# Performance work log

Hardware: AMD Instinct MI355X
Metric: run time of the kernel (lower is better)

The kernel has to match this reference:

```python
import jax, jax.numpy as jnp
import numpy as np

TEMPERATURE = 0.1
BASE_TEMPERATURE = 0.07
EPS = 1e-10


def setup_inputs() -> dict:
    key = jax.random.key(0)
    k1, k2 = jax.random.split(key)
    # feats_: [total_classes=64, n_view=128, feat_dim=256] sampled anchor features
    feats_ = jax.random.normal(k1, (64, 128, 256), dtype=jnp.float32)
    # labels_: class id per anchor group (21-class dataset -> repeats across groups)
    labels_ = jax.random.randint(k2, (64,), 0, 21, dtype=jnp.int32)
    return {"feats_": feats_, "labels_": labels_}


def reference(feats_, labels_):
    anchor_num, n_view, d = feats_.shape
    N = anchor_num * n_view
    # torch.cat(torch.unbind(feats_, dim=1), dim=0): view-major flattening
    cf = jnp.transpose(feats_, (1, 0, 2)).reshape(N, d)  # [N, d]
    # labels for the flattened ordering (mask.repeat tiles the [A,A] eq-mask)
    big_labels = jnp.tile(labels_, n_view)  # [N]

    logits = jnp.matmul(cf, cf.T) / TEMPERATURE  # [N, N]
    logits = logits - jax.lax.stop_gradient(jnp.max(logits, axis=1, keepdims=True))

    mask = (big_labels[:, None] == big_labels[None, :]).astype(jnp.float32)
    neg_mask = 1.0 - mask                       # negatives BEFORE removing diagonal
    mask = mask * (1.0 - jnp.eye(N, dtype=jnp.float32))  # positives exclude self

    exp_logits = jnp.exp(logits)
    neg_logits = jnp.sum(exp_logits * neg_mask, axis=1, keepdims=True)  # [N, 1]
    log_prob = logits - jnp.log(exp_logits + neg_logits + EPS)
    mean_log_prob_pos = jnp.sum(mask * log_prob, axis=1) / jnp.sum(mask, axis=1)
    loss = jnp.mean(-(TEMPERATURE / BASE_TEMPERATURE) * mean_log_prob_pos)
    return loss
```

## Files before the change

kernel.cpp:

```cpp
#include <hip/hip_runtime.h>
#include <hip/hip_bf16.h>

#define N_ROWS 8192
#define DIM 256
#define NANCH 64
#define NVIEW 128
#define NPART 8

typedef __attribute__((ext_vector_type(8))) short bf16x8;
typedef __attribute__((ext_vector_type(4))) float f32x4;
typedef __attribute__((ext_vector_type(16))) float f32x16;
typedef __attribute__((ext_vector_type(4))) float float4v;
typedef __attribute__((ext_vector_type(4))) unsigned short ushort4v;

__device__ __forceinline__ unsigned short f2bf(float x) {
  union { float f; unsigned int u; } c; c.f = x;
  unsigned int u = c.u;
  unsigned int r = (u + 0x7fffu + ((u >> 16) & 1u)) >> 16;
  return (unsigned short)r;
}

__device__ __forceinline__ float bf2f(unsigned short b) {
  union { unsigned int u; float f; } c; c.u = ((unsigned int)b) << 16;
  return c.f;
}

__device__ __forceinline__ void gload_lds16(const void* g, void* l) {
  __builtin_amdgcn_global_load_lds(
      (const __attribute__((address_space(1))) unsigned int*)g,
      (__attribute__((address_space(3))) unsigned int*)l, 16, 0, 0);
}

__global__ void cast_diag_kernel(const float4v* __restrict__ in,
                                 ushort4v* __restrict__ out,
                                 float* __restrict__ diag) {
  const int w = threadIdx.x >> 6;
  const int l = threadIdx.x & 63;
  const int row = blockIdx.x * 4 + w;
  const float s = 3.16227766016838f;
  float4v v = in[row * 64 + l];
  ushort4v o;
  o.x = f2bf(v.x * s);
  o.y = f2bf(v.y * s);
  o.z = f2bf(v.z * s);
  o.w = f2bf(v.w * s);
  out[row * 64 + l] = o;
  float c0 = bf2f(o.x), c1 = bf2f(o.y), c2 = bf2f(o.z), c3 = bf2f(o.w);
  float ss = c0 * c0 + c1 * c1 + c2 * c2 + c3 * c3;
#pragma unroll
  for (int st = 1; st < 64; st <<= 1) ss += __shfl_xor(ss, st);
  if (l == 0) diag[row] = ss;
}

__global__ __launch_bounds__(512, 2) void pcl_negsum(
    const unsigned short* __restrict__ Xb, const int* __restrict__ labels,
    const float* __restrict__ diag, float* __restrict__ ns_partial) {
  const int bx = blockIdx.x;
  const int rbp = bx & 31;
  const int part = bx >> 5;
  const int abase = part * 8;
  const int tid = threadIdx.x;
  const int wid = tid >> 6;
  const int lane = tid & 63;
  const int l31 = lane & 31;
  const int khalf = lane >> 5;
  const int rg = wid >> 1;
  const int cg = wid & 1;
  const int R0 = rbp * 256;

  __shared__ __align__(16) unsigned short ring[4 * 64 * DIM];
  __shared__ float sdiag[256];
  __shared__ float nsacc[256];
  __shared__ int slab[NANCH];

  if (tid < NANCH) slab[tid] = labels[tid];
  if (tid < 256) { sdiag[tid] = diag[R0 + tid]; nsacc[tid] = 0.f; }
  __syncthreads();
  const int myLab = slab[rbp * 2 + (rg >> 1)];

  bf16x8 afrag[2][16];
#pragma unroll
  for (int ri = 0; ri < 2; ++ri) {
#pragma unroll
    for (int ks = 0; ks < 16; ++ks) {
      const unsigned short* p =
          Xb + (size_t)(R0 + rg * 64 + ri * 32 + l31) * DIM + ks * 16 + khalf * 8;
      afrag[ri][ks] = *(const bf16x8*)p;
    }
  }
#pragma unroll
  for (int ri = 0; ri < 2; ++ri)
#pragma unroll
    for (int ks = 0; ks < 16; ++ks) asm volatile("" : "+v"(afrag[ri][ks]));

  float thr;
  {
    float d = sdiag[rg * 64 + lane];
#pragma unroll
    for (int st = 1; st < 64; st <<= 1) d = fminf(d, __shfl_xor(d, st));
    thr = d - 40.f;
  }

  char* const L0 = (char*)&ring[0];

#define STAGE(H)                                                                \
  do {                                                                          \
    const unsigned short* _s =                                                  \
        Xb + (size_t)((abase + ((H) >> 1)) * NVIEW + ((H) & 1) * 64 + lane) *   \
                 DIM + wid * 8;                                                 \
    char* _d = L0 + ((H) & 3) * 32768 + wid * 1024;                             \
    gload_lds16(_s, _d);                                                        \
    gload_lds16(_s + 64, _d + 8192);                                            \
    gload_lds16(_s + 128, _d + 16384);                                          \
    gload_lds16(_s + 192, _d + 24576);                                          \
  } while (0)

  STAGE(0);
  STAGE(1);
  STAGE(2);

#define ITER(S, VN)                                                             \
  do {                                                                          \
    if ((S) + 3 < 16) STAGE((S) + 3);                                           \
    asm volatile("s_waitcnt vmcnt(" #VN ")");                                   \
    __builtin_amdgcn_sched_barrier(0);                                          \
    __builtin_amdgcn_s_barrier();                                               \
    __builtin_amdgcn_sched_barrier(0);                                          \
    const char* _sb =                                                           \
        L0 + ((S) & 3) * 32768 + khalf * 1024 + cg * 512 + l31 * 16;            \
    f32x16 a0A = {}, a0B = {}, a1A = {}, a1B = {};                              \
    __builtin_amdgcn_s_setprio(1);                                              \
    _Pragma("unroll") for (int ks = 0; ks < 8; ++ks) {                          \
      bf16x8 b0 = *(const bf16x8*)(_sb + ks * 2048);                            \
      bf16x8 b1 = *(const bf16x8*)(_sb + (ks + 8) * 2048);                      \
      a0A = __builtin_amdgcn_mfma_f32_32x32x16_bf16(afrag[0][ks], b0, a0A, 0, 0, 0); \
      a1A = __builtin_amdgcn_mfma_f32_32x32x16_bf16(afrag[1][ks], b0, a1A, 0, 0, 0); \
      a0B = __builtin_amdgcn_mfma_f32_32x32x16_bf16(afrag[0][ks + 8], b1, a0B, 0, 0, 0); \
      a1B = __builtin_amdgcn_mfma_f32_32x32x16_bf16(afrag[1][ks + 8], b1, a1B, 0, 0, 0); \
    }                                                                           \
    __builtin_amdgcn_s_setprio(0);                                              \
    if (slab[abase + ((S) >> 1)] != myLab) {                                    \
      f32x16 c0 = a0A + a0B;                                                    \
      f32x16 c1 = a1A + a1B;                                                    \
      float vmax = fmaxf(c0[0], c1[0]);                                         \
      _Pragma("unroll") for (int r = 1; r < 16; ++r)                            \
          vmax = fmaxf(vmax, fmaxf(c0[r], c1[r]));                              \
      if (__builtin_expect(__any(vmax > thr), 0)) {                             \
        _Pragma("unroll") for (int t2 = 0; t2 < 2; ++t2) {                      \
          _Pragma("unroll") for (int r = 0; r < 16; ++r) {                      \
            const int rloc = (r & 3) + 8 * (r >> 2) + 4 * khalf;                \
            const int row = rg * 64 + t2 * 32 + rloc;                           \
            float v = t2 ? c1[r] : c0[r];                                       \
            float mr = sdiag[row];                                              \
            float e = (v > mr - 40.f) ? __expf(v - mr) : 0.f;                   \
            _Pragma("unroll") for (int st = 1; st < 32; st <<= 1)               \
                e += __shfl_xor(e, st);                                         \
            if (l31 == 0) atomicAdd(&nsacc[row], e);                            \
          }                                                                     \
        }                                                                       \
      }                                                                         \
    }                                                                           \
    __builtin_amdgcn_s_barrier();                                               \
  } while (0)

  ITER(0, 12);  ITER(1, 12);  ITER(2, 12);  ITER(3, 12);
  ITER(4, 12);  ITER(5, 12);  ITER(6, 12);  ITER(7, 12);
  ITER(8, 12);  ITER(9, 12);  ITER(10, 12); ITER(11, 12);
  ITER(12, 12); ITER(13, 8);  ITER(14, 4);  ITER(15, 0);

#undef ITER
#undef STAGE

  __syncthreads();
  if (tid < 256) ns_partial[part * N_ROWS + R0 + tid] = nsacc[tid];
}

__global__ __launch_bounds__(512, 4) void pcl_pos(
    const unsigned short* __restrict__ Xb, const int* __restrict__ labels,
    const float* __restrict__ diag, const float* __restrict__ ns_partial,
    float* __restrict__ partials) {
  const int blk = blockIdx.x;
  const int r0 = blk * 32;
  const int tid = threadIdx.x;
  const int wid = tid >> 6;
  const int lane = tid & 63;
  const int lo = lane & 15;
  const int hi = lane >> 4;
  const int cq = wid & 3;
  const int bq = wid >> 2;

  __shared__ int slab[NANCH];
  __shared__ float sred[8][32];
  __shared__ float smf[32];
  __shared__ float snsf[32];
  __shared__ float slog[32];
  __shared__ int poslist[NANCH];
  __shared__ int scnt;

  if (tid < NANCH) slab[tid] = labels[tid];
  if (tid >= 64 && tid < 96) {
    int r = tid - 64;
    smf[r] = diag[r0 + r];
    float s = 0.f;
#pragma unroll
    for (int p = 0; p < NPART; ++p) s += ns_partial[p * N_ROWS + r0 + r];
    snsf[r] = s;
    slog[r] = __logf(s + 1e-10f);
  }
  if (tid == 0) {
    int La0 = labels[blk >> 2];
    int c = 0;
    for (int b = 0; b < NANCH; ++b)
      if (labels[b] == La0) poslist[c++] = b;
    scnt = c;
  }
  __syncthreads();

  bf16x8 afrag[2][8];
#pragma unroll
  for (int ri = 0; ri < 2; ++ri) {
#pragma unroll
    for (int ks = 0; ks < 8; ++ks) {
      const unsigned short* p = Xb + (r0 + ri * 16 + lo) * DIM + ks * 32 + hi * 8;
      afrag[ri][ks] = *(const bf16x8*)p;
      asm volatile("" : "+v"(afrag[ri][ks]));
    }
  }

  const int cnt = scnt;
  float pos[8];
#pragma unroll
  for (int t = 0; t < 8; ++t) pos[t] = 0.f;

  for (int p = bq; p < cnt; p += 2) {
    const int b = poslist[p];
    const int c0 = b * NVIEW + cq * 32;
    f32x4 acc[2][2];
#pragma unroll
    for (int ri = 0; ri < 2; ++ri)
#pragma unroll
      for (int ci = 0; ci < 2; ++ci)
        acc[ri][ci] = (f32x4){0.f, 0.f, 0.f, 0.f};

#pragma unroll
    for (int ks = 0; ks < 8; ++ks) {
      bf16x8 b0 = *(const bf16x8*)(Xb + (c0 + lo) * DIM + ks * 32 + hi * 8);
      bf16x8 b1 = *(const bf16x8*)(Xb + (c0 + 16 + lo) * DIM + ks * 32 + hi * 8);
      acc[0][0] = __builtin_amdgcn_mfma_f32_16x16x32_bf16(afrag[0][ks], b0, acc[0][0], 0, 0, 0);
      acc[0][1] = __builtin_amdgcn_mfma_f32_16x16x32_bf16(afrag[0][ks], b1, acc[0][1], 0, 0, 0);
      acc[1][0] = __builtin_amdgcn_mfma_f32_16x16x32_bf16(afrag[1][ks], b0, acc[1][0], 0, 0, 0);
      acc[1][1] = __builtin_amdgcn_mfma_f32_16x16x32_bf16(afrag[1][ks], b1, acc[1][1], 0, 0, 0);
    }

#pragma unroll
    for (int ri = 0; ri < 2; ++ri) {
#pragma unroll
      for (int ci = 0; ci < 2; ++ci) {
#pragma unroll
        for (int reg = 0; reg < 4; ++reg) {
          const int t = ri * 4 + reg;
          const int row = ri * 16 + hi * 4 + reg;
          int grow = r0 + row;
          int gcol = c0 + ci * 16 + lo;
          if (grow != gcol) {
            float d = acc[ri][ci][reg] - smf[row];
            float lp;
            if (__builtin_expect(d > -45.f, 0))
              lp = d - __logf(__expf(d) + snsf[row] + 1e-10f);
            else
              lp = d - slog[row];
            pos[t] += lp;
          }
        }
      }
    }
  }

#pragma unroll
  for (int t = 0; t < 8; ++t) {
#pragma unroll
    for (int st = 1; st < 16; st <<= 1) pos[t] += __shfl_xor(pos[t], st);
  }
  if (lo == 0) {
#pragma unroll
    for (int ri = 0; ri < 2; ++ri)
#pragma unroll
      for (int reg = 0; reg < 4; ++reg)
        sred[wid][ri * 16 + hi * 4 + reg] = pos[ri * 4 + reg];
  }
  __syncthreads();

  const float poscnt = (float)(cnt * NVIEW - 1);
  if (tid < 32) {
    float P = 0.f;
#pragma unroll
    for (int w = 0; w < 8; ++w) P += sred[w][tid];
    smf[tid] = P / poscnt;
  }
  __syncthreads();
  if (tid == 0) {
    float s = 0.f;
    for (int r = 0; r < 32; ++r) s += smf[r];
    partials[blk] = s;
  }
}

__global__ void final_reduce(const float* __restrict__ partials, float* __restrict__ out) {
  __shared__ float s[256];
  int t = threadIdx.x;
  s[t] = partials[t];
  __syncthreads();
  for (int st = 128; st > 0; st >>= 1) {
    if (t < st) s[t] += s[t + st];
    __syncthreads();
  }
  if (t == 0) out[0] = -(0.1f / 0.07f) * s[0] / (float)N_ROWS;
}

extern "C" void kernel_launch(void* const* d_in, const int* in_sizes, int n_in,
                              void* d_out, int out_size, void* d_ws, size_t ws_size,
                              hipStream_t stream) {
  const float* feats = (const float*)d_in[0];
  const int* labels = (const int*)d_in[1];
  float* out = (float*)d_out;

  char* base = (char*)d_ws;
  unsigned short* Xb = (unsigned short*)d_ws;
  float* diag = (float*)(base + (size_t)N_ROWS * DIM * 2);
  float* ns_partial = (float*)(base + (size_t)N_ROWS * DIM * 2 + N_ROWS * 4);
  float* partials = (float*)(base + (size_t)N_ROWS * DIM * 2 + N_ROWS * 4 +
                             NPART * N_ROWS * 4);

  cast_diag_kernel<<<N_ROWS / 4, 256, 0, stream>>>((const float4v*)feats,
                                                   (ushort4v*)Xb, diag);
  pcl_negsum<<<32 * NPART, 512, 0, stream>>>(Xb, labels, diag, ns_partial);
  pcl_pos<<<N_ROWS / 32, 512, 0, stream>>>(Xb, labels, diag, ns_partial, partials);
  final_reduce<<<1, 256, 0, stream>>>(partials, out);
}
```

Before: 75.35 us.

## Fuse positive-pair log-prob sums into negsum pass and drop separate pos GEMM

The separate positive-pair kernel, which recomputed GEMM tiles, is removed. The negsum kernel now also accumulates, per row, the sum of logit differences over positive columns and the exp terms for hot positives. The mean log-prob is then rebuilt algebraically in a small combine kernel as (SD - npos*log(NS) - EP/NS)/npos, a first-order expansion of log(exp(d)+NS). Blocks shrink to 256 threads with a 2-stage LDS ring and 512 blocks. The EP/NS term approximates log(1+e/NS) and may lose accuracy when positives are hot relative to the negative sum.

```diff
diff --git a/kernel.cpp b/kernel.cpp
--- a/kernel.cpp
+++ b/kernel.cpp
@@ -8,7 +8,6 @@
 #define NPART 8
 
 typedef __attribute__((ext_vector_type(8))) short bf16x8;
-typedef __attribute__((ext_vector_type(4))) float f32x4;
 typedef __attribute__((ext_vector_type(16))) float f32x16;
 typedef __attribute__((ext_vector_type(4))) float float4v;
 typedef __attribute__((ext_vector_type(4))) unsigned short ushort4v;
@@ -52,12 +51,13 @@
   if (l == 0) diag[row] = ss;
 }
 
-__global__ __launch_bounds__(512, 2) void pcl_negsum(
+__global__ __launch_bounds__(256, 2) void pcl_negsum(
     const unsigned short* __restrict__ Xb, const int* __restrict__ labels,
-    const float* __restrict__ diag, float* __restrict__ ns_partial) {
+    const float* __restrict__ diag, float* __restrict__ ns_partial,
+    float* __restrict__ sd_partial, float* __restrict__ ep_partial) {
   const int bx = blockIdx.x;
-  const int rbp = bx & 31;
-  const int part = bx >> 5;
+  const int part = bx & 7;
+  const int rb = bx >> 3;
   const int abase = part * 8;
   const int tid = threadIdx.x;
   const int wid = tid >> 6;
@@ -66,17 +66,24 @@
   const int khalf = lane >> 5;
   const int rg = wid >> 1;
   const int cg = wid & 1;
-  const int R0 = rbp * 256;
-
-  __shared__ __align__(16) unsigned short ring[4 * 64 * DIM];
-  __shared__ float sdiag[256];
-  __shared__ float nsacc[256];
+  const int R0 = rb * 128;
+
+  __shared__ __align__(16) unsigned short ring[2 * 64 * DIM];
+  __shared__ float sdiag[128];
+  __shared__ float nsacc[128];
+  __shared__ float sdacc[128];
+  __shared__ float epacc[128];
   __shared__ int slab[NANCH];
 
   if (tid < NANCH) slab[tid] = labels[tid];
-  if (tid < 256) { sdiag[tid] = diag[R0 + tid]; nsacc[tid] = 0.f; }
-  __syncthreads();
-  const int myLab = slab[rbp * 2 + (rg >> 1)];
+  if (tid < 128) {
+    sdiag[tid] = diag[R0 + tid];
+    nsacc[tid] = 0.f;
+    sdacc[tid] = 0.f;
+    epacc[tid] = 0.f;
+  }
+  __syncthreads();
+  const int myLab = slab[rb];
 
   bf16x8 afrag[2][16];
 #pragma unroll
@@ -108,26 +115,21 @@
     const unsigned short* _s =                                                  \
         Xb + (size_t)((abase + ((H) >> 1)) * NVIEW + ((H) & 1) * 64 + lane) *   \
                  DIM + wid * 8;                                                 \
-    char* _d = L0 + ((H) & 3) * 32768 + wid * 1024;                             \
-    gload_lds16(_s, _d);                                                        \
-    gload_lds16(_s + 64, _d + 8192);                                            \
-    gload_lds16(_s + 128, _d + 16384);                                          \
-    gload_lds16(_s + 192, _d + 24576);                                          \
+    char* _d = L0 + ((H) & 1) * 32768 + wid * 1024;                             \
+    _Pragma("unroll") for (int i = 0; i < 8; ++i)                               \
+        gload_lds16(_s + i * 32, _d + i * 4096);                                \
   } while (0)
 
   STAGE(0);
-  STAGE(1);
-  STAGE(2);
-
-#define ITER(S, VN)                                                             \
+
+#define BODY(S, VNSTR)                                                          \
   do {                                                                          \
-    if ((S) + 3 < 16) STAGE((S) + 3);                                           \
-    asm volatile("s_waitcnt vmcnt(" #VN ")");                                   \
+    if ((S) + 1 < 16) STAGE((S) + 1);                                           \
+    asm volatile("s_waitcnt vmcnt(" VNSTR ")");                                 \
     __builtin_amdgcn_sched_barrier(0);                                          \
     __builtin_amdgcn_s_barrier();                                               \
     __builtin_amdgcn_sched_barrier(0);                                          \
-    const char* _sb =                                                           \
-        L0 + ((S) & 3) * 32768 + khalf * 1024 + cg * 512 + l31 * 16;            \
+    const char* _sb = L0 + ((S) & 1) * 32768 + khalf * 1024 + cg * 512 + l31 * 16; \
     f32x16 a0A = {}, a0B = {}, a1A = {}, a1B = {};                              \
     __builtin_amdgcn_s_setprio(1);                                              \
     _Pragma("unroll") for (int ks = 0; ks < 8; ++ks) {                          \
@@ -139,182 +141,126 @@
       a1B = __builtin_amdgcn_mfma_f32_32x32x16_bf16(afrag[1][ks + 8], b1, a1B, 0, 0, 0); \
     }                                                                           \
     __builtin_amdgcn_s_setprio(0);                                              \
-    if (slab[abase + ((S) >> 1)] != myLab) {                                    \
-      f32x16 c0 = a0A + a0B;                                                    \
-      f32x16 c1 = a1A + a1B;                                                    \
-      float vmax = fmaxf(c0[0], c1[0]);                                         \
-      _Pragma("unroll") for (int r = 1; r < 16; ++r)                            \
-          vmax = fmaxf(vmax, fmaxf(c0[r], c1[r]));                              \
-      if (__builtin_expect(__any(vmax > thr), 0)) {                             \
+    const bool is_pos = (slab[abase + ((S) >> 1)] == myLab);                    \
+    f32x16 c0 = a0A + a0B;                                                      \
+    f32x16 c1 = a1A + a1B;                                                      \
+    float vmax = fmaxf(c0[0], c1[0]);                                           \
+    _Pragma("unroll") for (int r = 1; r < 16; ++r)                              \
+        vmax = fmaxf(vmax, fmaxf(c0[r], c1[r]));                                \
+    const bool anyhot = __any(vmax > thr);                                      \
+    if (__builtin_expect(is_pos, 0)) {                                          \
+      if (!anyhot) {                                                            \
         _Pragma("unroll") for (int t2 = 0; t2 < 2; ++t2) {                      \
           _Pragma("unroll") for (int r = 0; r < 16; ++r) {                      \
             const int rloc = (r & 3) + 8 * (r >> 2) + 4 * khalf;                \
             const int row = rg * 64 + t2 * 32 + rloc;                           \
-            float v = t2 ? c1[r] : c0[r];                                       \
-            float mr = sdiag[row];                                              \
-            float e = (v > mr - 40.f) ? __expf(v - mr) : 0.f;                   \
+            float d = (t2 ? c1[r] : c0[r]) - sdiag[row];                        \
             _Pragma("unroll") for (int st = 1; st < 32; st <<= 1)               \
-                e += __shfl_xor(e, st);                                         \
-            if (l31 == 0) atomicAdd(&nsacc[row], e);                            \
+                d += __shfl_xor(d, st);                                         \
+            if (l31 == 0) atomicAdd(&sdacc[row], d);                            \
           }                                                                     \
+        }                                                                       \
+      } else {                                                                  \
+        const bool dt = (abase + ((S) >> 1)) == rb;                             \
+        _Pragma("unroll") for (int t2 = 0; t2 < 2; ++t2) {                      \
+          _Pragma("unroll") for (int r = 0; r < 16; ++r) {                      \
+            const int rloc = (r & 3) + 8 * (r >> 2) + 4 * khalf;                \
+            const int row = rg * 64 + t2 * 32 + rloc;                           \
+            const int cl = ((S) & 1) * 64 + cg * 32 + l31;                      \
+            const bool isdiag = dt && (row == cl);                              \
+            float v = (t2 ? c1[r] : c0[r]);                                     \
+            float d = v - sdiag[row];                                           \
+            float sd_e = isdiag ? 0.f : d;                                      \
+            float e = (!isdiag && d > -40.f) ? __expf(d) : 0.f;                 \
+            _Pragma("unroll") for (int st = 1; st < 32; st <<= 1) {             \
+              sd_e += __shfl_xor(sd_e, st);                                     \
+              e += __shfl_xor(e, st);                                           \
+            }                                                                   \
+            if (l31 == 0) {                                                     \
+              atomicAdd(&sdacc[row], sd_e);                                     \
+              if (e != 0.f) atomicAdd(&epacc[row], e);                          \
+            }                                                                   \
+          }                                                                     \
+        }                                                                       \
+      }                                                                         \
+    } else if (__builtin_expect(anyhot, 0)) {                                   \
+      _Pragma("unroll") for (int t2 = 0; t2 < 2; ++t2) {                        \
+        _Pragma("unroll") for (int r = 0; r < 16; ++r) {                        \
+          const int rloc = (r & 3) + 8 * (r >> 2) + 4 * khalf;                  \
+          const int row = rg * 64 + t2 * 32 + rloc;                             \
+          float d = (t2 ? c1[r] : c0[r]) - sdiag[row];                          \
+          float e = (d > -40.f) ? __expf(d) : 0.f;                              \
+          _Pragma("unroll") for (int st = 1; st < 32; st <<= 1)                 \
+              e += __shfl_xor(e, st);                                           \
+          if (l31 == 0) atomicAdd(&nsacc[row], e);                              \
         }                                                                       \
       }                                                                         \
     }                                                                           \
     __builtin_amdgcn_s_barrier();                                               \
   } while (0)
 
-  ITER(0, 12);  ITER(1, 12);  ITER(2, 12);  ITER(3, 12);
-  ITER(4, 12);  ITER(5, 12);  ITER(6, 12);  ITER(7, 12);
-  ITER(8, 12);  ITER(9, 12);  ITER(10, 12); ITER(11, 12);
-  ITER(12, 12); ITER(13, 8);  ITER(14, 4);  ITER(15, 0);
-
-#undef ITER
+  BODY(0, "8");  BODY(1, "8");  BODY(2, "8");  BODY(3, "8");
+  BODY(4, "8");  BODY(5, "8");  BODY(6, "8");  BODY(7, "8");
+  BODY(8, "8");  BODY(9, "8");  BODY(10, "8"); BODY(11, "8");
+  BODY(12, "8"); BODY(13, "8"); BODY(14, "8"); BODY(15, "0");
+
+#undef BODY
 #undef STAGE
 
   __syncthreads();
-  if (tid < 256) ns_partial[part * N_ROWS + R0 + tid] = nsacc[tid];
-}
-
-__global__ __launch_bounds__(512, 4) void pcl_pos(
-    const unsigned short* __restrict__ Xb, const int* __restrict__ labels,
-    const float* __restrict__ diag, const float* __restrict__ ns_partial,
-    float* __restrict__ partials) {
-  const int blk = blockIdx.x;
-  const int r0 = blk * 32;
+  if (tid < 128) {
+    ns_partial[part * N_ROWS + R0 + tid] = nsacc[tid];
+    sd_partial[part * N_ROWS + R0 + tid] = sdacc[tid];
+    ep_partial[part * N_ROWS + R0 + tid] = epacc[tid];
+  }
+}
+
+__global__ void pcl_combine(const int* __restrict__ labels,
+                            const float* __restrict__ ns_partial,
+                            const float* __restrict__ sd_partial,
+                            const float* __restrict__ ep_partial,
+                            float* __restrict__ partials) {
   const int tid = threadIdx.x;
-  const int wid = tid >> 6;
-  const int lane = tid & 63;
-  const int lo = lane & 15;
-  const int hi = lane >> 4;
-  const int cq = wid & 3;
-  const int bq = wid >> 2;
-
+  const int row = blockIdx.x * 256 + tid;
   __shared__ int slab[NANCH];
-  __shared__ float sred[8][32];
-  __shared__ float smf[32];
-  __shared__ float snsf[32];
-  __shared__ float slog[32];
-  __shared__ int poslist[NANCH];
-  __shared__ int scnt;
-
+  __shared__ float sred[256];
   if (tid < NANCH) slab[tid] = labels[tid];
-  if (tid >= 64 && tid < 96) {
-    int r = tid - 64;
-    smf[r] = diag[r0 + r];
-    float s = 0.f;
-#pragma unroll
-    for (int p = 0; p < NPART; ++p) s += ns_partial[p * N_ROWS + r0 + r];
-    snsf[r] = s;
-    slog[r] = __logf(s + 1e-10f);
-  }
-  if (tid == 0) {
-    int La0 = labels[blk >> 2];
-    int c = 0;
-    for (int b = 0; b < NANCH; ++b)
-      if (labels[b] == La0) poslist[c++] = b;
-    scnt = c;
-  }
-  __syncthreads();
-
-  bf16x8 afrag[2][8];
-#pragma unroll
-  for (int ri = 0; ri < 2; ++ri) {
-#pragma unroll
-    for (int ks = 0; ks < 8; ++ks) {
-      const unsigned short* p = Xb + (r0 + ri * 16 + lo) * DIM + ks * 32 + hi * 8;
-      afrag[ri][ks] = *(const bf16x8*)p;
-      asm volatile("" : "+v"(afrag[ri][ks]));
-    }
-  }
-
-  const int cnt = scnt;
-  float pos[8];
-#pragma unroll
-  for (int t = 0; t < 8; ++t) pos[t] = 0.f;
-
-  for (int p = bq; p < cnt; p += 2) {
-    const int b = poslist[p];
-    const int c0 = b * NVIEW + cq * 32;
-    f32x4 acc[2][2];
-#pragma unroll
-    for (int ri = 0; ri < 2; ++ri)
-#pragma unroll
-      for (int ci = 0; ci < 2; ++ci)
-        acc[ri][ci] = (f32x4){0.f, 0.f, 0.f, 0.f};
-
-#pragma unroll
-    for (int ks = 0; ks < 8; ++ks) {
-      bf16x8 b0 = *(const bf16x8*)(Xb + (c0 + lo) * DIM + ks * 32 + hi * 8);
-      bf16x8 b1 = *(const bf16x8*)(Xb + (c0 + 16 + lo) * DIM + ks * 32 + hi * 8);
-      acc[0][0] = __builtin_amdgcn_mfma_f32_16x16x32_bf16(afrag[0][ks], b0, acc[0][0], 0, 0, 0);
-      acc[0][1] = __builtin_amdgcn_mfma_f32_16x16x32_bf16(afrag[0][ks], b1, acc[0][1], 0, 0, 0);
-      acc[1][0] = __builtin_amdgcn_mfma_f32_16x16x32_bf16(afrag[1][ks], b0, acc[1][0], 0, 0, 0);
-      acc[1][1] = __builtin_amdgcn_mfma_f32_16x16x32_bf16(afrag[1][ks], b1, acc[1][1], 0, 0, 0);
-    }
-
-#pragma unroll
-    for (int ri = 0; ri < 2; ++ri) {
-#pragma unroll
-      for (int ci = 0; ci < 2; ++ci) {
-#pragma unroll
-        for (int reg = 0; reg < 4; ++reg) {
-          const int t = ri * 4 + reg;
-          const int row = ri * 16 + hi * 4 + reg;
-          int grow = r0 + row;
-          int gcol = c0 + ci * 16 + lo;
-          if (grow != gcol) {
-            float d = acc[ri][ci][reg] - smf[row];
-            float lp;
-            if (__builtin_expect(d > -45.f, 0))
-              lp = d - __logf(__expf(d) + snsf[row] + 1e-10f);
-            else
-              lp = d - slog[row];
-            pos[t] += lp;
-          }
-        }
-      }
-    }
-  }
-
-#pragma unroll
-  for (int t = 0; t < 8; ++t) {
-#pragma unroll
-    for (int st = 1; st < 16; st <<= 1) pos[t] += __shfl_xor(pos[t], st);
-  }
-  if (lo == 0) {
-#pragma unroll
-    for (int ri = 0; ri < 2; ++ri)
-#pragma unroll
-      for (int reg = 0; reg < 4; ++reg)
-        sred[wid][ri * 16 + hi * 4 + reg] = pos[ri * 4 + reg];
-  }
-  __syncthreads();
-
-  const float poscnt = (float)(cnt * NVIEW - 1);
-  if (tid < 32) {
-    float P = 0.f;
-#pragma unroll
-    for (int w = 0; w < 8; ++w) P += sred[w][tid];
-    smf[tid] = P / poscnt;
-  }
-  __syncthreads();
-  if (tid == 0) {
-    float s = 0.f;
-    for (int r = 0; r < 32; ++r) s += smf[r];
-    partials[blk] = s;
-  }
+  __syncthreads();
+
+  const int lab = slab[row >> 7];
+  int cnt = 0;
+#pragma unroll
+  for (int b = 0; b < NANCH; ++b) cnt += (slab[b] == lab) ? 1 : 0;
+
+  float NS = 0.f, SD = 0.f, EP = 0.f;
+#pragma unroll
+  for (int p = 0; p < NPART; ++p) {
+    NS += ns_partial[p * N_ROWS + row];
+    SD += sd_partial[p * N_ROWS + row];
+    EP += ep_partial[p * N_ROWS + row];
+  }
+  const float npos = (float)(cnt * NVIEW - 1);
+  const float nse = NS + 1e-10f;
+  const float mlpp = (SD - npos * __logf(nse) - EP / nse) / npos;
+  sred[tid] = mlpp;
+  __syncthreads();
+  for (int st = 128; st > 0; st >>= 1) {
+    if (tid < st) sred[tid] += sred[tid + st];
+    __syncthreads();
+  }
+  if (tid == 0) partials[blockIdx.x] = sred[0];
 }
 
 __global__ void final_reduce(const float* __restrict__ partials, float* __restrict__ out) {
-  __shared__ float s[256];
+  __shared__ float s[32];
   int t = threadIdx.x;
-  s[t] = partials[t];
-  __syncthreads();
-  for (int st = 128; st > 0; st >>= 1) {
-    if (t < st) s[t] += s[t + st];
-    __syncthreads();
-  }
-  if (t == 0) out[0] = -(0.1f / 0.07f) * s[0] / (float)N_ROWS;
+  if (t < 32) s[t] = partials[t];
+  __syncthreads();
+  if (t == 0) {
+    float sum = 0.f;
+    for (int r = 0; r < 32; ++r) sum += s[r];
+    out[0] = -(0.1f / 0.07f) * sum / (float)N_ROWS;
+  }
 }
 
 extern "C" void kernel_launch(void* const* d_in, const int* in_sizes, int n_in,
@@ -326,14 +272,18 @@
 
   char* base = (char*)d_ws;
   unsigned short* Xb = (unsigned short*)d_ws;
-  float* diag = (float*)(base + (size_t)N_ROWS * DIM * 2);
-  float* ns_partial = (float*)(base + (size_t)N_ROWS * DIM * 2 + N_ROWS * 4);
-  float* partials = (float*)(base + (size_t)N_ROWS * DIM * 2 + N_ROWS * 4 +
-                             NPART * N_ROWS * 4);
+  size_t off = (size_t)N_ROWS * DIM * 2;
+  float* diag = (float*)(base + off);       off += N_ROWS * 4;
+  float* ns_partial = (float*)(base + off); off += NPART * N_ROWS * 4;
+  float* sd_partial = (float*)(base + off); off += NPART * N_ROWS * 4;
+  float* ep_partial = (float*)(base + off); off += NPART * N_ROWS * 4;
+  float* partials = (float*)(base + off);
 
   cast_diag_kernel<<<N_ROWS / 4, 256, 0, stream>>>((const float4v*)feats,
                                                    (ushort4v*)Xb, diag);
-  pcl_negsum<<<32 * NPART, 512, 0, stream>>>(Xb, labels, diag, ns_partial);
-  pcl_pos<<<N_ROWS / 32, 512, 0, stream>>>(Xb, labels, diag, ns_partial, partials);
-  final_reduce<<<1, 256, 0, stream>>>(partials, out);
-}
+  pcl_negsum<<<NANCH * NPART, 256, 0, stream>>>(Xb, labels, diag, ns_partial,
+                                                sd_partial, ep_partial);
+  pcl_combine<<<N_ROWS / 256, 256, 0, stream>>>(labels, ns_partial, sd_partial,
+                                                ep_partial, partials);
+  final_reduce<<<1, 64, 0, stream>>>(partials, out);
+}
```

New measurement: 93.78 us. 1.24x slower.
